# Kernel optimization log

Hardware: AMD Instinct MI355X
Metric: run time of the kernel (lower is better)

## Reference

```python
import jax, jax.numpy as jnp
import numpy as np
from jax import lax

THRESHOLD = 0.9


def _conv(x, w, b, stride):
    # x: [B,C,H,W], w: [O,I,3,3] (OIHW)
    y = lax.conv_general_dilated(x, w, (stride, stride), 'SAME',
                                 dimension_numbers=('NCHW', 'OIHW', 'NCHW'))
    return y + b[None, :, None, None]


def _expert(x, w1, b1, w2, b2, wf, bf):
    h = jax.nn.relu(_conv(x, w1, b1, 2))   # [B,64,112,112]
    h = jax.nn.relu(_conv(h, w2, b2, 2))   # [B,128,56,56]
    g = h.mean(axis=(2, 3))                # [B,128] global average pool
    return g @ wf + bf                     # [B,2] logits


def setup_inputs() -> dict:
    key = jax.random.key(0)
    ks = jax.random.split(key, 13)
    f32 = jnp.float32
    def rn(k, shape, scale):
        return jax.random.normal(k, shape, dtype=f32) * scale
    return {
        'x':    rn(ks[0], (64, 3, 224, 224), 1.0),
        't_w1': rn(ks[1], (64, 3, 3, 3),   0.2),
        't_b1': jnp.zeros((64,), f32),
        't_w2': rn(ks[2], (128, 64, 3, 3), 0.05),
        't_b2': jnp.zeros((128,), f32),
        't_wf': rn(ks[3], (128, 2),        0.1),
        't_bf': jnp.zeros((2,), f32),
        'f_w1': rn(ks[4], (64, 3, 3, 3),   0.2),
        'f_b1': jnp.zeros((64,), f32),
        'f_w2': rn(ks[5], (128, 64, 3, 3), 0.05),
        'f_b2': jnp.zeros((128,), f32),
        'f_wf': rn(ks[6], (128, 2),        0.1),
        'f_bf': jnp.zeros((2,), f32),
    }


def reference(x, t_w1, t_b1, t_w2, t_b2, t_wf, t_bf,
              f_w1, f_b1, f_w2, f_b2, f_wf, f_bf):
    t_logits = _expert(x, t_w1, t_b1, t_w2, t_b2, t_wf, t_bf)   # [B,2]
    t_conf = jax.nn.softmax(t_logits, axis=1).max(axis=1)        # [B]
    use_texture2 = t_conf <= THRESHOLD                           # [B] bool
    # jit-friendly dense evaluation of the second expert; the where-mask
    # reproduces the original gather/scatter blend exactly (values and grads).
    f_logits = _expert(x, f_w1, f_b1, f_w2, f_b2, f_wf, f_bf)   # [B,2]
    output = jnp.where(use_texture2[:, None],
                       0.7 * t_logits + 0.3 * f_logits,
                       t_logits)
    freq_usage = use_texture2.astype(jnp.float32).mean()
    return (output, freq_usage)
```

## Files before the change

kernel.cpp:

```cpp
#include <hip/hip_runtime.h>
#include <hip/hip_fp16.h>
#include <math.h>


#define W2B_OFF   0ull
#define W1F_OFF   294912ull
#define G_OFF     303104ull
#define H1_OFF    368640ull
#define H1E_US    52301824ull
#define H1B_US    817216ull
#define WS_NEED   (H1_OFF + 2ull*H1E_US*2ull + 4096ull)

typedef __attribute__((ext_vector_type(8))) short bf16x8;
typedef __attribute__((ext_vector_type(8))) _Float16 half8;
typedef __attribute__((ext_vector_type(4))) float f32x4;

__device__ inline ushort f2h(float v) {
  __half h = __float2half(v);
  return *(ushort*)&h;
}

__global__ __launch_bounds__(256) void prep_new(
    const float* __restrict__ w2_t, const float* __restrict__ w2_f,
    const float* __restrict__ w1_t, const float* __restrict__ w1_f,
    char* __restrict__ ws) {
  int idx = blockIdx.x * 256 + threadIdx.x;
  ushort* w2frag = (ushort*)(ws + W2B_OFF);
  ushort* w1frag = (ushort*)(ws + W1F_OFF);
  if (idx < 147456) {
    int j    = idx & 7;
    int lane = (idx >> 3) & 63;
    int t2   = idx >> 9;
    int kc   = t2 % 18;
    int t3   = t2 / 18;
    int octile = t3 & 7;
    int e    = t3 >> 3;
    int oc = octile * 16 + (lane & 15);
    int kk = kc * 32 + (lane >> 4) * 8 + j;
    int kh = kk / 192, r2 = kk - kh * 192, kw = r2 >> 6, slot = r2 & 63;
    int icp = ((slot >> 2) & 3) * 16 + ((slot >> 4) & 3) * 4 + (slot & 3);
    const float* src = e ? w2_f : w2_t;
    w2frag[idx] = f2h(src[((oc * 64 + icp) * 3 + kh) * 3 + kw]);
  } else if (idx < 147456 + 4096) {
    int i2   = idx - 147456;
    int j    = i2 & 7;
    int lane = (i2 >> 3) & 63;
    int m    = (i2 >> 9) & 3;
    int e    = (i2 >> 11) & 1;
    int oc = m * 16 + (lane & 15);
    int kk = (lane >> 4) * 8 + j;
    const float* src = e ? w1_f : w1_t;
    w1frag[i2] = f2h((kk < 27) ? src[oc * 27 + kk] : 0.f);
  }
}

__global__ __launch_bounds__(256) void conv1_mfma(
    const float* __restrict__ x,
    const ushort* __restrict__ w1f_all,
    const float* __restrict__ b1_t, const float* __restrict__ b1_f,
    ushort* __restrict__ h1_all)
{
  const int gR  = blockIdx.x;
  const int b   = blockIdx.y;
  const int e   = blockIdx.z;
  const int tid = threadIdx.x;
  const int w    = tid >> 6;
  const int lane = tid & 63;
  const int q    = lane >> 4;
  const int n    = lane & 15;

  ushort* h1b = h1_all + (size_t)e * H1E_US + (size_t)b * H1B_US;
  const float* b1 = e ? b1_f : b1_t;

  constexpr int CW = 233;
  __shared__ unsigned int xs[3 * 9 * CW];

  const float* xb = x + (size_t)b * 150528;
  const int xr0 = 8 * gR;
  for (int i = tid; i < 1512; i += 256) {
    int ic  = i / 504;
    int rem = i - ic * 504;
    int r   = rem / 56;
    int u   = rem - r * 56;
    int xr  = xr0 + r;
    float4 p = make_float4(0.f, 0.f, 0.f, 0.f);
    if (xr < 224) p = *(const float4*)(xb + (ic * 224 + xr) * 224 + 4 * u);
    int base = (ic * 9 + r) * CW + 4 * u;
    xs[base + 0] = (unsigned int)f2h(p.x);
    xs[base + 1] = (unsigned int)f2h(p.y);
    xs[base + 2] = (unsigned int)f2h(p.z);
    xs[base + 3] = (unsigned int)f2h(p.w);
  }
  if (tid < 27) xs[tid * CW + 224] = 0;

  h1b[((size_t)((4 * gR + (tid >> 6)) * 113 + 112)) * 64 + (tid & 63)] = 0;
  if (gR == 0) {
    unsigned int* z = (unsigned int*)&h1b[(size_t)112 * 113 * 64];
    for (int i = tid; i < 3616; i += 256) z[i] = 0;
  }

  half8 wf[4];
#pragma unroll
  for (int m = 0; m < 4; ++m)
    wf[m] = *(const half8*)&w1f_all[(((size_t)(e * 4 + m)) * 64 + lane) * 8];
  float4 bv[4];
#pragma unroll
  for (int m = 0; m < 4; ++m)
    bv[m] = *(const float4*)&b1[m * 16 + 4 * q];

  int off[8];
#pragma unroll
  for (int j = 0; j < 8; ++j) {
    int kk = q * 8 + j;
    if (kk < 27) {
      int ic = kk / 9;
      int r9 = kk - ic * 9;
      int kh = r9 / 3;
      int kw = r9 - kh * 3;
      off[j] = (ic * 9 + kh) * CW + kw;
    } else {
      off[j] = -1;
    }
  }

  __syncthreads();

  const int row   = 4 * gR + w;
  const int rbase = (2 * w) * CW;

  for (int nt = 0; nt < 7; ++nt) {
    const int c = nt * 16 + n;
    const int base = rbase + 2 * c;
    unsigned int g[8];
#pragma unroll
    for (int j = 0; j < 8; ++j)
      g[j] = (off[j] >= 0) ? xs[base + off[j]] : 0u;
    union { half8 h; unsigned int u[4]; } bh;
#pragma unroll
    for (int p = 0; p < 4; ++p)
      bh.u[p] = (g[2 * p] & 0xffffu) | (g[2 * p + 1] << 16);
    f32x4 acc[4];
#pragma unroll
    for (int m = 0; m < 4; ++m) acc[m] = (f32x4){0.f, 0.f, 0.f, 0.f};
#pragma unroll
    for (int m = 0; m < 4; ++m)
      acc[m] = __builtin_amdgcn_mfma_f32_16x16x32_f16(wf[m], bh.h, acc[m], 0, 0, 0);
    size_t po = ((size_t)(row * 113 + c)) * 64 + q * 16;
    union { ushort us[16]; uint4 v4[2]; } pk;
#pragma unroll
    for (int m = 0; m < 4; ++m) {
      pk.us[m * 4 + 0] = f2h(fmaxf(acc[m][0] + bv[m].x, 0.f));
      pk.us[m * 4 + 1] = f2h(fmaxf(acc[m][1] + bv[m].y, 0.f));
      pk.us[m * 4 + 2] = f2h(fmaxf(acc[m][2] + bv[m].z, 0.f));
      pk.us[m * 4 + 3] = f2h(fmaxf(acc[m][3] + bv[m].w, 0.f));
    }
    *(uint4*)&h1b[po]     = pk.v4[0];
    *(uint4*)&h1b[po + 8] = pk.v4[1];
  }
}

__global__ __launch_bounds__(256, 2) void conv2_mfma(
    const ushort* __restrict__ h1_all,
    const ushort* __restrict__ w2frag,
    const float* __restrict__ b2_t, const float* __restrict__ b2_f,
    float* __restrict__ g)
{
  const int T = blockIdx.x;
  const int b = blockIdx.y;
  const int e = blockIdx.z;
  const int tid  = threadIdx.x;
  const int w    = tid >> 6;
  const int lane = tid & 63;
  const ushort* h1b = h1_all + (size_t)e * H1E_US + (size_t)b * H1B_US;
  const float* b2 = e ? b2_f : b2_t;

  __shared__ ushort hs[5 * 113 * 64];

  const int q   = lane >> 4;
  const int n   = lane & 15;
  const int pxl = lane & 7;
  const int rl  = (lane >> 3) & 1;

  half8 afr[2][18];
#pragma unroll
  for (int mt = 0; mt < 2; ++mt)
#pragma unroll
    for (int kc = 0; kc < 18; ++kc)
      afr[mt][kc] = *(const half8*)
          &w2frag[((size_t)((e * 8 + 2 * w + mt) * 18 + kc)) * 512 + lane * 8];

#pragma unroll
  for (int half = 0; half < 2; ++half) {
    bf16x8 tmp[9];
    int dst[9];
    bool ok[9];
#pragma unroll
    for (int k = 0; k < 9; ++k) {
      int s = tid + (half * 9 + k) * 256;
      ok[k] = (s < 4520);
      int r = s / 904;
      int rem = s - 904 * r;
      int hx = rem >> 3, gq = rem & 7;
      if (ok[k])
        tmp[k] = *(const bf16x8*)&h1b[((size_t)((4 * T + r) * 113 + hx)) * 64 + 8 * gq];
      dst[k] = (r * 113 + hx) * 64 + 8 * (gq ^ (hx & 7));
    }
#pragma unroll
    for (int k = 0; k < 9; ++k)
      if (ok[k]) *(bf16x8*)&hs[dst[k]] = tmp[k];
  }
  __syncthreads();

  f32x4 acc[2][7];
#pragma unroll
  for (int mt = 0; mt < 2; ++mt)
#pragma unroll
    for (int nt = 0; nt < 7; ++nt) acc[mt][nt] = (f32x4){0.f, 0.f, 0.f, 0.f};

#pragma unroll
  for (int kh = 0; kh < 3; ++kh) {
    const int rbase = (kh + 2 * rl) * 113 * 64;
#pragma unroll
    for (int kw = 0; kw < 3; ++kw) {
#pragma unroll
      for (int icc = 0; icc < 2; ++icc) {
        const int kc = kh * 6 + kw * 2 + icc;
        const int gsw = 8 * ((icc * 4 + q) ^ ((2 * pxl + kw) & 7));
        half8 bf[7];
#pragma unroll
        for (int nt = 0; nt < 7; ++nt) {
          int hx = 2 * (8 * nt + pxl) + kw;
          bf[nt] = *(const half8*)&hs[rbase + hx * 64 + gsw];
        }
#pragma unroll
        for (int mt = 0; mt < 2; ++mt) {
#pragma unroll
          for (int nt = 0; nt < 7; ++nt)
            acc[mt][nt] = __builtin_amdgcn_mfma_f32_16x16x32_f16(
                afr[mt][kc], bf[nt], acc[mt][nt], 0, 0, 0);
        }
      }
    }
  }

#pragma unroll
  for (int mt = 0; mt < 2; ++mt) {
#pragma unroll
    for (int reg = 0; reg < 4; ++reg) {
      const int oc = 32 * w + 16 * mt + 4 * q + reg;
      const float bias = b2[oc];
      float s = 0.f;
#pragma unroll
      for (int nt = 0; nt < 7; ++nt) s += fmaxf(acc[mt][nt][reg] + bias, 0.f);
      s += __shfl_xor(s, 1);
      s += __shfl_xor(s, 2);
      s += __shfl_xor(s, 4);
      s += __shfl_xor(s, 8);
      if (n == 0) atomicAdd(&g[((size_t)e * 64 + b) * 128 + oc], s);
    }
  }
}

__global__ __launch_bounds__(64) void finale(
    const float* __restrict__ g,
    const float* __restrict__ t_wf, const float* __restrict__ t_bf,
    const float* __restrict__ f_wf, const float* __restrict__ f_bf,
    float* __restrict__ out)
{
  const int b = threadIdx.x;
  const float inv = 1.0f / 3136.0f;
  const float* gt = g + b * 128;
  const float* gf = g + (64 + b) * 128;
  float lt0 = t_bf[0], lt1 = t_bf[1];
  float lf0 = f_bf[0], lf1 = f_bf[1];
  for (int k = 0; k < 128; ++k) {
    float vt = gt[k] * inv;
    float vf = gf[k] * inv;
    lt0 = fmaf(vt, t_wf[2 * k],     lt0);
    lt1 = fmaf(vt, t_wf[2 * k + 1], lt1);
    lf0 = fmaf(vf, f_wf[2 * k],     lf0);
    lf1 = fmaf(vf, f_wf[2 * k + 1], lf1);
  }
  float m  = fmaxf(lt0, lt1);
  float e0 = expf(lt0 - m), e1 = expf(lt1 - m);
  float conf = fmaxf(e0, e1) / (e0 + e1);
  bool use2 = (conf <= 0.9f);
  out[2 * b]     = use2 ? 0.7f * lt0 + 0.3f * lf0 : lt0;
  out[2 * b + 1] = use2 ? 0.7f * lt1 + 0.3f * lf1 : lt1;
  unsigned long long mask = __ballot(use2);
  if (b == 0) out[128] = (float)__popcll(mask) * (1.0f / 64.0f);
}

__global__ __launch_bounds__(256) void transpose_w2(
    const float* __restrict__ w2_t, const float* __restrict__ w2_f,
    float* __restrict__ w2t) {
  int idx = blockIdx.x * 256 + threadIdx.x;
  int e = idx / 73728;
  int r = idx - e * 73728;
  int k = r >> 7, oc = r & 127;
  const float* src = e ? w2_f : w2_t;
  w2t[idx] = src[oc * 576 + k];
}

__global__ __launch_bounds__(256, 3) void fused_expert(
    const float* __restrict__ x,
    const float* __restrict__ w1_t, const float* __restrict__ b1_t,
    const float* __restrict__ b2_t,
    const float* __restrict__ w1_f, const float* __restrict__ b1_f,
    const float* __restrict__ b2_f,
    const float* __restrict__ w2t_all, float* __restrict__ g)
{
  const int tile = blockIdx.x, b = blockIdx.y, e = blockIdx.z;
  const int ty = tile >> 1, tx = tile & 1;
  const float* w1  = e ? w1_f : w1_t;
  const float* b1  = e ? b1_f : b1_t;
  const float* b2  = e ? b2_f : b2_t;
  const float* w2t = w2t_all + e * 73728;
  __shared__ float x_s[3 * 19 * 116];
  __shared__ float h1_s[8 * 9 * 58];
  __shared__ float w1_s[1728];
  const int tid = threadIdx.x;
  {
    const float* xb = x + (size_t)b * 150528;
    const int xr0 = ty * 16, xc0 = tx * 112;
    for (int idx = tid; idx < 3 * 19 * 116; idx += 256) {
      int ic = idx / (19 * 116);
      int rem = idx - ic * (19 * 116);
      int r = rem / 116, cc = rem - r * 116;
      int xr = xr0 + r, xc = xc0 + cc;
      float v = 0.f;
      if (xr < 224 && xc < 224 && cc < 115) v = xb[(ic * 224 + xr) * 224 + xc];
      x_s[idx] = v;
    }
    for (int idx = tid; idx < 1728; idx += 256) w1_s[idx] = w1[idx];
  }
  const int ocg = tid >> 4, posg = tid & 15;
  int pbase[7];
#pragma unroll
  for (int j = 0; j < 7; ++j) {
    int p = posg + 16 * j, py = p / 28, px = p - py * 28;
    pbase[j] = py * 2 * 58 + px * 2;
  }
  float acc[7][8];
#pragma unroll
  for (int j = 0; j < 7; ++j)
#pragma unroll
    for (int i = 0; i < 8; ++i) acc[j][i] = 0.f;
  const int hc_l = tid >> 5, l32 = tid & 31;
  for (int c = 0; c < 8; ++c) {
    __syncthreads();
    {
      const int hc = c * 8 + hc_l;
      const float bias = b1[hc];
      float wr[27];
#pragma unroll
      for (int qq = 0; qq < 27; ++qq) wr[qq] = w1_s[hc * 27 + qq];
      for (int p = l32; p < 513; p += 32) {
        int hy = p / 57, hx = p - hy * 57;
        float a = bias;
#pragma unroll
        for (int ic = 0; ic < 3; ++ic)
#pragma unroll
          for (int kh = 0; kh < 3; ++kh) {
            const float* row = &x_s[ic * (19 * 116) + (2 * hy + kh) * 116 + 2 * hx];
            a = fmaf(row[0], wr[ic * 9 + kh * 3 + 0], a);
            a = fmaf(row[1], wr[ic * 9 + kh * 3 + 1], a);
            a = fmaf(row[2], wr[ic * 9 + kh * 3 + 2], a);
          }
        float v = fmaxf(a, 0.f);
        int hy_g = ty * 8 + hy, hx_g = tx * 56 + hx;
        if (hy_g >= 112 || hx_g >= 112) v = 0.f;
        h1_s[hc_l * 522 + hy * 58 + hx] = v;
      }
    }
    __syncthreads();
    for (int ic_l = 0; ic_l < 8; ++ic_l) {
#pragma unroll
      for (int kh = 0; kh < 3; ++kh)
#pragma unroll
        for (int kw = 0; kw < 3; ++kw) {
          const int k = (c * 8 + ic_l) * 9 + kh * 3 + kw;
          const float4 wA = *(const float4*)(w2t + k * 128 + ocg * 8);
          const float4 wB = *(const float4*)(w2t + k * 128 + ocg * 8 + 4);
          const float* hp = &h1_s[ic_l * 522 + kh * 58 + kw];
#pragma unroll
          for (int j = 0; j < 7; ++j) {
            float h = hp[pbase[j]];
            acc[j][0] = fmaf(wA.x, h, acc[j][0]);
            acc[j][1] = fmaf(wA.y, h, acc[j][1]);
            acc[j][2] = fmaf(wA.z, h, acc[j][2]);
            acc[j][3] = fmaf(wA.w, h, acc[j][3]);
            acc[j][4] = fmaf(wB.x, h, acc[j][4]);
            acc[j][5] = fmaf(wB.y, h, acc[j][5]);
            acc[j][6] = fmaf(wB.z, h, acc[j][6]);
            acc[j][7] = fmaf(wB.w, h, acc[j][7]);
          }
        }
    }
  }
  __syncthreads();
  float* red = x_s;
#pragma unroll
  for (int i = 0; i < 8; ++i) {
    float bb = b2[ocg * 8 + i];
    float t = 0.f;
#pragma unroll
    for (int j = 0; j < 7; ++j) t += fmaxf(acc[j][i] + bb, 0.f);
    red[posg * 129 + ocg * 8 + i] = t;
  }
  __syncthreads();
  if (tid < 128) {
    float t = 0.f;
#pragma unroll
    for (int pg = 0; pg < 16; ++pg) t += red[pg * 129 + tid];
    atomicAdd(&g[(e * 64 + b) * 128 + tid], t);
  }
}

extern "C" void kernel_launch(void* const* d_in, const int* in_sizes, int n_in,
                              void* d_out, int out_size, void* d_ws, size_t ws_size,
                              hipStream_t stream) {
  const float* x    = (const float*)d_in[0];
  const float* t_w1 = (const float*)d_in[1];
  const float* t_b1 = (const float*)d_in[2];
  const float* t_w2 = (const float*)d_in[3];
  const float* t_b2 = (const float*)d_in[4];
  const float* t_wf = (const float*)d_in[5];
  const float* t_bf = (const float*)d_in[6];
  const float* f_w1 = (const float*)d_in[7];
  const float* f_b1 = (const float*)d_in[8];
  const float* f_w2 = (const float*)d_in[9];
  const float* f_b2 = (const float*)d_in[10];
  const float* f_wf = (const float*)d_in[11];
  const float* f_bf = (const float*)d_in[12];
  float* out = (float*)d_out;
  char* ws = (char*)d_ws;

  if (ws_size >= WS_NEED) {
    float*  gbuf   = (float*)(ws + G_OFF);
    ushort* h1     = (ushort*)(ws + H1_OFF);
    ushort* w2frag = (ushort*)(ws + W2B_OFF);
    ushort* w1f    = (ushort*)(ws + W1F_OFF);
    hipMemsetAsync(gbuf, 0, 2 * 64 * 128 * sizeof(float), stream);
    prep_new<<<592, 256, 0, stream>>>(t_w2, f_w2, t_w1, f_w1, ws);
    conv1_mfma<<<dim3(28, 64, 2), 256, 0, stream>>>(x, w1f, t_b1, f_b1, h1);
    conv2_mfma<<<dim3(28, 64, 2), 256, 0, stream>>>(h1, w2frag, t_b2, f_b2, gbuf);
    finale<<<1, 64, 0, stream>>>(gbuf, t_wf, t_bf, f_wf, f_bf, out);
  } else {
    float* w2t = (float*)ws;
    float* g2  = (float*)(ws + 589824);
    hipMemsetAsync(g2, 0, 2 * 64 * 128 * sizeof(float), stream);
    transpose_w2<<<576, 256, 0, stream>>>(t_w2, f_w2, w2t);
    fused_expert<<<dim3(28, 64, 2), 256, 0, stream>>>(
        x, t_w1, t_b1, t_b2, f_w1, f_b1, f_b2, w2t, g2);
    finale<<<1, 64, 0, stream>>>(g2, t_wf, t_bf, f_wf, f_bf, out);
  }
}
```

Measured before the change: 239.6 us.

## Fuse conv1 into conv2 kernel, computing halo rows of h1 in shared memory

Merges the separate conv1 and conv2 kernels into one kernel that computes the five conv1 output rows each conv2 tile needs, including one halo row, directly into LDS. This removes the large fp16 h1 intermediate round-trip through global memory and one kernel launch. In exchange, each block recomputes the overlapping conv1 row, adds a second LDS buffer for the input tile, and is restricted to one block per CU through the launch bounds.

New measurement: 318.6 us. 33.0% more time.

```diff
diff --git a/kernel.cpp b/kernel.cpp
--- a/kernel.cpp
+++ b/kernel.cpp
@@ -6,10 +6,7 @@
 #define W2B_OFF   0ull
 #define W1F_OFF   294912ull
 #define G_OFF     303104ull
-#define H1_OFF    368640ull
-#define H1E_US    52301824ull
-#define H1B_US    817216ull
-#define WS_NEED   (H1_OFF + 2ull*H1E_US*2ull + 4096ull)
+#define WS_NEED   (G_OFF + 65536ull + 4096ull)
 
 typedef __attribute__((ext_vector_type(8))) short bf16x8;
 typedef __attribute__((ext_vector_type(8))) _Float16 half8;
@@ -54,132 +51,30 @@
   }
 }
 
-__global__ __launch_bounds__(256) void conv1_mfma(
+__global__ __launch_bounds__(256, 1) void fused12(
     const float* __restrict__ x,
     const ushort* __restrict__ w1f_all,
+    const ushort* __restrict__ w2frag,
     const float* __restrict__ b1_t, const float* __restrict__ b1_f,
-    ushort* __restrict__ h1_all)
-{
-  const int gR  = blockIdx.x;
-  const int b   = blockIdx.y;
-  const int e   = blockIdx.z;
-  const int tid = threadIdx.x;
-  const int w    = tid >> 6;
-  const int lane = tid & 63;
-  const int q    = lane >> 4;
-  const int n    = lane & 15;
-
-  ushort* h1b = h1_all + (size_t)e * H1E_US + (size_t)b * H1B_US;
-  const float* b1 = e ? b1_f : b1_t;
-
-  constexpr int CW = 233;
-  __shared__ unsigned int xs[3 * 9 * CW];
-
-  const float* xb = x + (size_t)b * 150528;
-  const int xr0 = 8 * gR;
-  for (int i = tid; i < 1512; i += 256) {
-    int ic  = i / 504;
-    int rem = i - ic * 504;
-    int r   = rem / 56;
-    int u   = rem - r * 56;
-    int xr  = xr0 + r;
-    float4 p = make_float4(0.f, 0.f, 0.f, 0.f);
-    if (xr < 224) p = *(const float4*)(xb + (ic * 224 + xr) * 224 + 4 * u);
-    int base = (ic * 9 + r) * CW + 4 * u;
-    xs[base + 0] = (unsigned int)f2h(p.x);
-    xs[base + 1] = (unsigned int)f2h(p.y);
-    xs[base + 2] = (unsigned int)f2h(p.z);
-    xs[base + 3] = (unsigned int)f2h(p.w);
-  }
-  if (tid < 27) xs[tid * CW + 224] = 0;
-
-  h1b[((size_t)((4 * gR + (tid >> 6)) * 113 + 112)) * 64 + (tid & 63)] = 0;
-  if (gR == 0) {
-    unsigned int* z = (unsigned int*)&h1b[(size_t)112 * 113 * 64];
-    for (int i = tid; i < 3616; i += 256) z[i] = 0;
-  }
-
-  half8 wf[4];
-#pragma unroll
-  for (int m = 0; m < 4; ++m)
-    wf[m] = *(const half8*)&w1f_all[(((size_t)(e * 4 + m)) * 64 + lane) * 8];
-  float4 bv[4];
-#pragma unroll
-  for (int m = 0; m < 4; ++m)
-    bv[m] = *(const float4*)&b1[m * 16 + 4 * q];
-
-  int off[8];
-#pragma unroll
-  for (int j = 0; j < 8; ++j) {
-    int kk = q * 8 + j;
-    if (kk < 27) {
-      int ic = kk / 9;
-      int r9 = kk - ic * 9;
-      int kh = r9 / 3;
-      int kw = r9 - kh * 3;
-      off[j] = (ic * 9 + kh) * CW + kw;
-    } else {
-      off[j] = -1;
-    }
-  }
-
-  __syncthreads();
-
-  const int row   = 4 * gR + w;
-  const int rbase = (2 * w) * CW;
-
-  for (int nt = 0; nt < 7; ++nt) {
-    const int c = nt * 16 + n;
-    const int base = rbase + 2 * c;
-    unsigned int g[8];
-#pragma unroll
-    for (int j = 0; j < 8; ++j)
-      g[j] = (off[j] >= 0) ? xs[base + off[j]] : 0u;
-    union { half8 h; unsigned int u[4]; } bh;
-#pragma unroll
-    for (int p = 0; p < 4; ++p)
-      bh.u[p] = (g[2 * p] & 0xffffu) | (g[2 * p + 1] << 16);
-    f32x4 acc[4];
-#pragma unroll
-    for (int m = 0; m < 4; ++m) acc[m] = (f32x4){0.f, 0.f, 0.f, 0.f};
-#pragma unroll
-    for (int m = 0; m < 4; ++m)
-      acc[m] = __builtin_amdgcn_mfma_f32_16x16x32_f16(wf[m], bh.h, acc[m], 0, 0, 0);
-    size_t po = ((size_t)(row * 113 + c)) * 64 + q * 16;
-    union { ushort us[16]; uint4 v4[2]; } pk;
-#pragma unroll
-    for (int m = 0; m < 4; ++m) {
-      pk.us[m * 4 + 0] = f2h(fmaxf(acc[m][0] + bv[m].x, 0.f));
-      pk.us[m * 4 + 1] = f2h(fmaxf(acc[m][1] + bv[m].y, 0.f));
-      pk.us[m * 4 + 2] = f2h(fmaxf(acc[m][2] + bv[m].z, 0.f));
-      pk.us[m * 4 + 3] = f2h(fmaxf(acc[m][3] + bv[m].w, 0.f));
-    }
-    *(uint4*)&h1b[po]     = pk.v4[0];
-    *(uint4*)&h1b[po + 8] = pk.v4[1];
-  }
-}
-
-__global__ __launch_bounds__(256, 2) void conv2_mfma(
-    const ushort* __restrict__ h1_all,
-    const ushort* __restrict__ w2frag,
     const float* __restrict__ b2_t, const float* __restrict__ b2_f,
     float* __restrict__ g)
 {
-  const int T = blockIdx.x;
+  const int U = blockIdx.x;
   const int b = blockIdx.y;
   const int e = blockIdx.z;
   const int tid  = threadIdx.x;
   const int w    = tid >> 6;
   const int lane = tid & 63;
-  const ushort* h1b = h1_all + (size_t)e * H1E_US + (size_t)b * H1B_US;
+  const int q    = lane >> 4;
+  const int n    = lane & 15;
+  const int pxl  = lane & 7;
+  const int rl   = (lane >> 3) & 1;
+
+  __shared__ ushort hs[5 * 113 * 64];
+  __shared__ ushort xs[3 * 11 * 228];
+
+  const float* b1 = e ? b1_f : b1_t;
   const float* b2 = e ? b2_f : b2_t;
-
-  __shared__ ushort hs[5 * 113 * 64];
-
-  const int q   = lane >> 4;
-  const int n   = lane & 15;
-  const int pxl = lane & 7;
-  const int rl  = (lane >> 3) & 1;
 
   half8 afr[2][18];
 #pragma unroll
@@ -189,25 +84,73 @@
       afr[mt][kc] = *(const half8*)
           &w2frag[((size_t)((e * 8 + 2 * w + mt) * 18 + kc)) * 512 + lane * 8];
 
-#pragma unroll
-  for (int half = 0; half < 2; ++half) {
-    bf16x8 tmp[9];
-    int dst[9];
-    bool ok[9];
-#pragma unroll
-    for (int k = 0; k < 9; ++k) {
-      int s = tid + (half * 9 + k) * 256;
-      ok[k] = (s < 4520);
-      int r = s / 904;
-      int rem = s - 904 * r;
-      int hx = rem >> 3, gq = rem & 7;
-      if (ok[k])
-        tmp[k] = *(const bf16x8*)&h1b[((size_t)((4 * T + r) * 113 + hx)) * 64 + 8 * gq];
-      dst[k] = (r * 113 + hx) * 64 + 8 * (gq ^ (hx & 7));
-    }
-#pragma unroll
-    for (int k = 0; k < 9; ++k)
-      if (ok[k]) *(bf16x8*)&hs[dst[k]] = tmp[k];
+  half8 wf[4];
+#pragma unroll
+  for (int m = 0; m < 4; ++m)
+    wf[m] = *(const half8*)&w1f_all[(((size_t)(e * 4 + m)) * 64 + lane) * 8];
+  float4 bv1[4];
+#pragma unroll
+  for (int m = 0; m < 4; ++m)
+    bv1[m] = *(const float4*)&b1[m * 16 + 4 * q];
+
+  const float* xb = x + (size_t)b * 150528;
+  for (int i = tid; i < 1848; i += 256) {
+    int ic  = i / 616;
+    int rem = i - ic * 616;
+    int r   = rem / 56;
+    int u   = rem - r * 56;
+    int xr  = 8 * U + r;
+    float4 p = make_float4(0.f, 0.f, 0.f, 0.f);
+    if (xr < 224) p = *(const float4*)(xb + (ic * 224 + xr) * 224 + 4 * u);
+    uint2 uu;
+    uu.x = (unsigned int)f2h(p.x) | ((unsigned int)f2h(p.y) << 16);
+    uu.y = (unsigned int)f2h(p.z) | ((unsigned int)f2h(p.w) << 16);
+    *(uint2*)&xs[(ic * 11 + r) * 228 + 4 * u] = uu;
+  }
+  if (tid < 33) *(unsigned int*)&xs[tid * 228 + 224] = 0;
+  if (tid < 40) {
+    uint4 z = make_uint4(0, 0, 0, 0);
+    *(uint4*)&hs[((tid >> 3) * 113 + 112) * 64 + 8 * (tid & 7)] = z;
+  }
+  __syncthreads();
+
+  int off1[8];
+#pragma unroll
+  for (int j = 0; j < 8; ++j) {
+    int kk = q * 8 + j;
+    if (kk < 27) {
+      int ic = kk / 9, r9 = kk - 9 * ic, kh = r9 / 3, kw = r9 - 3 * kh;
+      off1[j] = (ic * 11 + kh) * 228 + kw;
+    } else {
+      off1[j] = -1;
+    }
+  }
+  for (int t = w; t < 35; t += 4) {
+    int s  = t / 7, nt = t - 7 * s;
+    int c  = 16 * nt + n;
+    int bo = 456 * s + 2 * c;
+    union { half8 h; ushort us[8]; } bh;
+#pragma unroll
+    for (int j = 0; j < 8; ++j)
+      bh.us[j] = (off1[j] >= 0) ? xs[off1[j] + bo] : (ushort)0;
+    f32x4 a1[4];
+#pragma unroll
+    for (int m = 0; m < 4; ++m) a1[m] = (f32x4){0.f, 0.f, 0.f, 0.f};
+#pragma unroll
+    for (int m = 0; m < 4; ++m)
+      a1[m] = __builtin_amdgcn_mfma_f32_16x16x32_f16(wf[m], bh.h, a1[m], 0, 0, 0);
+    const bool live = (4 * U + s) < 112;
+    union { ushort us[16]; uint4 v4[2]; } pk;
+#pragma unroll
+    for (int m = 0; m < 4; ++m) {
+      pk.us[m * 4 + 0] = f2h(live ? fmaxf(a1[m][0] + bv1[m].x, 0.f) : 0.f);
+      pk.us[m * 4 + 1] = f2h(live ? fmaxf(a1[m][1] + bv1[m].y, 0.f) : 0.f);
+      pk.us[m * 4 + 2] = f2h(live ? fmaxf(a1[m][2] + bv1[m].z, 0.f) : 0.f);
+      pk.us[m * 4 + 3] = f2h(live ? fmaxf(a1[m][3] + bv1[m].w, 0.f) : 0.f);
+    }
+    int colb = (s * 113 + c) * 64;
+    *(uint4*)&hs[colb + 8 * ((2 * q)     ^ (c & 7))] = pk.v4[0];
+    *(uint4*)&hs[colb + 8 * ((2 * q + 1) ^ (c & 7))] = pk.v4[1];
   }
   __syncthreads();
 
@@ -438,13 +381,12 @@
 
   if (ws_size >= WS_NEED) {
     float*  gbuf   = (float*)(ws + G_OFF);
-    ushort* h1     = (ushort*)(ws + H1_OFF);
     ushort* w2frag = (ushort*)(ws + W2B_OFF);
     ushort* w1f    = (ushort*)(ws + W1F_OFF);
     hipMemsetAsync(gbuf, 0, 2 * 64 * 128 * sizeof(float), stream);
     prep_new<<<592, 256, 0, stream>>>(t_w2, f_w2, t_w1, f_w1, ws);
-    conv1_mfma<<<dim3(28, 64, 2), 256, 0, stream>>>(x, w1f, t_b1, f_b1, h1);
-    conv2_mfma<<<dim3(28, 64, 2), 256, 0, stream>>>(h1, w2frag, t_b2, f_b2, gbuf);
+    fused12<<<dim3(28, 64, 2), 256, 0, stream>>>(
+        x, w1f, w2frag, t_b1, f_b1, t_b2, f_b2, gbuf);
     finale<<<1, 64, 0, stream>>>(gbuf, t_wf, t_bf, f_wf, f_bf, out);
   } else {
     float* w2t = (float*)ws;
```
